# Kernel tuning notes

Measured on AMD Instinct MI355X. Metric: run time of the kernel, lower is better.

Reference implementation:

```python
import jax, jax.numpy as jnp
import numpy as np
from jax import lax

B, L, D, H, NW, NL = 4, 256, 768, 384, 4, 9
WINDOWS = (3, 5, 7, 9)


def setup_inputs() -> dict:
    key = jax.random.key(0)
    ks = jax.random.split(key, 12)
    s = 0.05
    return {
        "seq_out": jax.random.normal(ks[0], (B, L, D), jnp.float32),
        "valid_ids": jax.random.randint(ks[1], (B, L), 0, 2),
        "w_ih_f": jax.random.normal(ks[2], (NW, 4 * H, D), jnp.float32) * s,
        "w_hh_f": jax.random.normal(ks[3], (NW, 4 * H, H), jnp.float32) * s,
        "b_ih_f": jax.random.normal(ks[4], (NW, 4 * H), jnp.float32) * s,
        "b_hh_f": jax.random.normal(ks[5], (NW, 4 * H), jnp.float32) * s,
        "w_ih_b": jax.random.normal(ks[6], (NW, 4 * H, D), jnp.float32) * s,
        "w_hh_b": jax.random.normal(ks[7], (NW, 4 * H, H), jnp.float32) * s,
        "b_ih_b": jax.random.normal(ks[8], (NW, 4 * H), jnp.float32) * s,
        "b_hh_b": jax.random.normal(ks[9], (NW, 4 * H), jnp.float32) * s,
        "lin_w": jax.random.normal(ks[10], (NL, D), jnp.float32) * s,
        "lin_b": jnp.zeros((NL,), jnp.float32),
    }


def _lstm_last(win, mask, W_ih, W_hh, b, reverse):
    # invalid (out-of-range) steps leave the state untouched, so the final
    # carry equals the hidden state after the last valid step (PyTorch LSTM math).
    Bx, Lx, w, Dx = win.shape
    Hh = W_hh.shape[1]

    def step(carry, xm):
        h, c = carry
        x_t, m = xm  # [B,L,D], [L]
        gates = x_t @ W_ih.T + h @ W_hh.T + b  # [B,L,4H], gate order i,f,g,o
        i, f, g, o = jnp.split(gates, 4, axis=-1)
        i = jax.nn.sigmoid(i)
        f = jax.nn.sigmoid(f)
        g = jnp.tanh(g)
        o = jax.nn.sigmoid(o)
        c_new = f * c + i * g
        h_new = o * jnp.tanh(c_new)
        m3 = m[None, :, None]
        return (jnp.where(m3, h_new, h), jnp.where(m3, c_new, c)), None

    init = (jnp.zeros((Bx, Lx, Hh), win.dtype), jnp.zeros((Bx, Lx, Hh), win.dtype))
    (h, _), _ = lax.scan(step, init, (jnp.moveaxis(win, 2, 0), mask.T), reverse=reverse)
    return h


def _window_features(x, w, Wif, Whf, bf, Wib, Whb, bb):
    # Faithful vectorization of windows_sequence: the sorted index_list for
    # position i is the contiguous slice [max(0,i-w//2) .. min(L-1,i+w//2)].
    Bx, Lx, Dx = x.shape
    half = w // 2
    pos = jnp.arange(Lx)[:, None] + jnp.arange(-half, half + 1)[None, :]  # [L,w]
    mask = (pos >= 0) & (pos < Lx)
    idx = jnp.clip(pos, 0, Lx - 1)
    win = x[:, idx, :]  # [B,L,w,D]
    h_f = _lstm_last(win, mask, Wif, Whf, bf, reverse=False)  # fwd dir: last output
    h_b = _lstm_last(win, mask, Wib, Whb, bb, reverse=True)   # bwd dir over reversed window
    return jnp.concatenate([h_f, h_b], axis=-1)  # [B,L,D]


def _valid_scatter(x, valid_ids):
    # Left-pack tokens with valid_ids==1 (the nested Python scatter loop).
    Bx, Lx, Dx = x.shape
    v = valid_ids.astype(jnp.int32)
    dest = jnp.where(v == 1, jnp.cumsum(v, axis=1) - 1, Lx)  # invalid -> pad slot

    def pack(row_x, row_d):
        return jnp.zeros((Lx + 1, Dx), row_x.dtype).at[row_d].set(row_x)[:Lx]

    return jax.vmap(pack)(x, dest)


def reference(seq_out, valid_ids, w_ih_f, w_hh_f, b_ih_f, b_hh_f,
              w_ih_b, w_hh_b, b_ih_b, b_hh_b, lin_w, lin_b):
    x = _valid_scatter(seq_out, valid_ids)  # [B,L,D]; dropout is identity in eval
    locals_ = [
        _window_features(x, WINDOWS[i],
                         w_ih_f[i], w_hh_f[i], b_ih_f[i] + b_hh_f[i],
                         w_ih_b[i], w_hh_b[i], b_ih_b[i] + b_hh_b[i])
        for i in range(NW)
    ]
    muti = jnp.stack(locals_, axis=2)  # [B,L,NW,D]
    # dot-att: query is the (packed) sequence output itself
    attn = jax.nn.softmax(
        jnp.einsum('bld,blwd->blw', x, muti) / jnp.sqrt(jnp.float32(D)), axis=-1)
    local_feat = jnp.einsum('blw,blwd->bld', attn, muti)
    out = x + local_feat
    return out @ lin_w.T + lin_b  # logits [B,L,NL]
```

## Files before the change

kernel.cpp:

```cpp
#include <hip/hip_runtime.h>
#include <math.h>

#define LL 256
#define DD 768
#define HH 384
#define G4 1536
#define NWIN 4
#define NLIN 9
#define NPOS 1024
#define PROJ_N 12288
#define HSTRIDE 520

typedef __attribute__((ext_vector_type(8))) short short8;
typedef __attribute__((ext_vector_type(4))) short short4v;
typedef __attribute__((ext_vector_type(16))) float f32x16;

static __device__ __forceinline__ float bf2f(unsigned short u) {
    union { unsigned int i; float f; } v; v.i = ((unsigned int)u) << 16; return v.f;
}
static __device__ __forceinline__ unsigned short f2bf(float f) {
    unsigned int u = __float_as_uint(f);
    u += 0x7fff + ((u >> 16) & 1);
    return (unsigned short)(u >> 16);
}
static __device__ __forceinline__ float fsig(float x) {
    return __builtin_amdgcn_rcpf(1.f + __expf(-x));
}
static __device__ __forceinline__ float ftanh(float x) {
    return 1.f - 2.f * __builtin_amdgcn_rcpf(1.f + __expf(2.f * x));
}

__global__ void zero_f4(float4* __restrict__ p, int n4) {
    int i = blockIdx.x * blockDim.x + threadIdx.x;
    if (i < n4) p[i] = make_float4(0.f, 0.f, 0.f, 0.f);
}

__global__ void scatter_kernel(const float* __restrict__ seq,
                               const int* __restrict__ valid,
                               unsigned short* __restrict__ xfrag) {
    const int b = blockIdx.x >> 5;
    const int chunk = blockIdx.x & 31;
    const int tid = threadIdx.x;
    __shared__ int vbuf[LL];
    __shared__ int dest[LL];
    vbuf[tid] = valid[b * LL + tid];
    __syncthreads();
    if (tid == 0) {
        int c = 0;
        for (int l = 0; l < LL; ++l) dest[l] = vbuf[l] ? c++ : -1;
    }
    __syncthreads();
    for (int l = chunk * 8; l < chunk * 8 + 8; ++l) {
        const int d = dest[l];
        if (d >= 0) {
            const float* src = seq + (size_t)(b * LL + l) * DD;
            const int pos = b * LL + d;
            const int pt = pos >> 5, pl = pos & 31;
            for (int j = tid; j < DD / 8; j += 256) {
                const float4 v0 = ((const float4*)src)[2 * j];
                const float4 v1 = ((const float4*)src)[2 * j + 1];
                short8 pv;
                pv[0] = (short)f2bf(v0.x); pv[1] = (short)f2bf(v0.y);
                pv[2] = (short)f2bf(v0.z); pv[3] = (short)f2bf(v0.w);
                pv[4] = (short)f2bf(v1.x); pv[5] = (short)f2bf(v1.y);
                pv[6] = (short)f2bf(v1.z); pv[7] = (short)f2bf(v1.w);
                *(short8*)(xfrag + ((size_t)(pt * 48 + (j >> 1)) * 512 + (pl + 32 * (j & 1)) * 8)) = pv;
            }
        }
    }
}

__global__ __launch_bounds__(256) void cast_frag(
        const float* __restrict__ srcF, const float* __restrict__ srcB,
        unsigned short* __restrict__ dst, int K) {
    __shared__ unsigned short lds[32 * 768];
    const int tid = threadIdx.x;
    const int vrow0 = blockIdx.x * 32;
    const int chain = vrow0 / G4;
    const int dir = chain >> 2, wi = chain & 3;
    const float* src = (dir ? srcB : srcF) + (size_t)(wi * G4 + (vrow0 % G4)) * K;
    const int total = 32 * K;
    for (int i = tid * 4; i < total; i += 1024) {
        const float4 v = *(const float4*)(src + i);
        lds[i + 0] = f2bf(v.x); lds[i + 1] = f2bf(v.y);
        lds[i + 2] = f2bf(v.z); lds[i + 3] = f2bf(v.w);
    }
    __syncthreads();
    const int nks = K >> 4;
    for (int slot = tid; slot < nks * 64; slot += 256) {
        const int ks = slot >> 6;
        const int lane = slot & 63;
        const int row = lane & 31;
        const int kb = ks * 16 + (lane >> 5) * 8;
        const short8 v = *(const short8*)&lds[row * K + kb];
        *(short8*)(dst + ((size_t)blockIdx.x * nks + ks) * 512 + lane * 8) = v;
    }
}

__global__ __launch_bounds__(256) void proj_mfma(
        const unsigned short* __restrict__ xf,
        const unsigned short* __restrict__ wf,
        const float* __restrict__ bihf, const float* __restrict__ bhhf,
        const float* __restrict__ bihb, const float* __restrict__ bhhb,
        unsigned short* __restrict__ proj) {
    __shared__ __align__(16) unsigned short st[4 * 4096];
    const int wv = threadIdx.x >> 6;
    const int lane = threadIdx.x & 63;
    const int colid = lane & 31, hq = lane >> 5;
    const int chain = blockIdx.x & 7;
    const int r8 = blockIdx.x >> 3;
    const int us = r8 % 12;
    const int mtg = r8 / 12;
    const int dir = chain >> 2, wi = chain & 3;

    const unsigned short* bP = wf + (size_t)((chain * 48 + wv * 12 + us) * 48) * 512 + lane * 8;
    const unsigned short* aP = xf + (size_t)(mtg * 4 * 48) * 512 + lane * 8;

    f32x16 acc[4] = {};
#pragma unroll 4
    for (int ks = 0; ks < 48; ++ks) {
        const short8 bv = *(const short8*)(bP + ks * 512);
        const short8 a0 = *(const short8*)(aP + (0 * 48 + ks) * 512);
        const short8 a1 = *(const short8*)(aP + (1 * 48 + ks) * 512);
        const short8 a2 = *(const short8*)(aP + (2 * 48 + ks) * 512);
        const short8 a3 = *(const short8*)(aP + (3 * 48 + ks) * 512);
        acc[0] = __builtin_amdgcn_mfma_f32_32x32x16_bf16(a0, bv, acc[0], 0, 0, 0);
        acc[1] = __builtin_amdgcn_mfma_f32_32x32x16_bf16(a1, bv, acc[1], 0, 0, 0);
        acc[2] = __builtin_amdgcn_mfma_f32_32x32x16_bf16(a2, bv, acc[2], 0, 0, 0);
        acc[3] = __builtin_amdgcn_mfma_f32_32x32x16_bf16(a3, bv, acc[3], 0, 0, 0);
    }
    const int br = wv * HH + us * 32 + colid;
    const float bv = (dir ? bihb : bihf)[wi * G4 + br] + (dir ? bhhb : bhhf)[wi * G4 + br];
#pragma unroll
    for (int i = 0; i < 4; ++i) {
#pragma unroll
        for (int r = 0; r < 16; ++r) {
            const int row = (r & 3) + 8 * (r >> 2) + 4 * hq;
            st[i * 4096 + (row * 32 + colid) * 4 + wv] = f2bf(acc[i][r] + bv);
        }
    }
    __syncthreads();
#pragma unroll
    for (int j = 0; j < 8; ++j) {
        const int idx = j * 256 + threadIdx.x;
        const int i = idx >> 9, rem = idx & 511;
        const int pl = rem >> 4, q = rem & 15;
        const int pos = (mtg * 4 + i) * 32 + pl;
        *(int4*)(proj + (size_t)pos * PROJ_N + chain * G4 + us * 128 + q * 8) =
            ((const int4*)st)[idx];
    }
}

__global__ __launch_bounds__(768, 3) void lstm_fused(
        const unsigned short* __restrict__ Wf,
        const unsigned short* __restrict__ proj,
        unsigned short* __restrict__ hfin) {
    const int chain = blockIdx.x & 7;
    const int pt = blockIdx.x >> 3;
    const int dir = chain >> 2, wi = chain & 3;
    const int w = 3 + 2 * wi, half = wi + 1;
    const int tid = threadIdx.x;
    const int lane = tid & 63, wv = tid >> 6;
    const int colid = lane & 31, hq = lane >> 5;
    const int uu = wv * 32 + colid;
    const int m0 = pt * 32, b = m0 >> 8, l0 = m0 & 255;

    __shared__ __align__(16) unsigned short Hbuf[2][24 * HSTRIDE];
    float c[16];
#pragma unroll
    for (int r = 0; r < 16; ++r) c[r] = 0.f;

    const unsigned short* projb = proj + (size_t)(b * LL) * PROJ_N + chain * G4 + uu * 4;
    const unsigned short* Wb = Wf + (size_t)((chain * 48 + wv) * 24) * 512 + lane * 8;
    const int ksp = uu >> 4, khp = (uu >> 3) & 1, jp = uu & 7;
    const int hslot = ksp * HSTRIDE + khp * 256 + jp;

    for (int s = 0; s < w; ++s) {
        const int t = dir ? (w - 1 - s) : s;
        const int tmh = t - half;
        unsigned short* cur = Hbuf[s & 1];
        const unsigned short* prev = Hbuf[(s & 1) ^ 1];

        short4v pj[16];
#pragma unroll
        for (int r = 0; r < 16; ++r) {
            const int row = (r & 3) + 8 * (r >> 2) + 4 * hq;
            int src = l0 + row + tmh;
            src = src < 0 ? 0 : (src > LL - 1 ? LL - 1 : src);
            pj[r] = __builtin_nontemporal_load((const short4v*)(projb + src * PROJ_N));
        }

        f32x16 acc0 = {}, acc1 = {}, acc2 = {}, acc3 = {};
        if (s > 0) {
            const unsigned short* Alds = prev + lane * 8;
#pragma unroll 4
            for (int ks = 0; ks < 24; ++ks) {
                const short8 av  = *(const short8*)(Alds + ks * HSTRIDE);
                const short8 bv0 = *(const short8*)(Wb + (size_t)(0 * 288 + ks) * 512);
                const short8 bv1 = *(const short8*)(Wb + (size_t)(1 * 288 + ks) * 512);
                const short8 bv2 = *(const short8*)(Wb + (size_t)(2 * 288 + ks) * 512);
                const short8 bv3 = *(const short8*)(Wb + (size_t)(3 * 288 + ks) * 512);
                acc0 = __builtin_amdgcn_mfma_f32_32x32x16_bf16(av, bv0, acc0, 0, 0, 0);
                acc1 = __builtin_amdgcn_mfma_f32_32x32x16_bf16(av, bv1, acc1, 0, 0, 0);
                acc2 = __builtin_amdgcn_mfma_f32_32x32x16_bf16(av, bv2, acc2, 0, 0, 0);
                acc3 = __builtin_amdgcn_mfma_f32_32x32x16_bf16(av, bv3, acc3, 0, 0, 0);
            }
        }

#pragma unroll
        for (int r = 0; r < 16; ++r) {
            const int row = (r & 3) + 8 * (r >> 2) + 4 * hq;
            const int src = l0 + row + tmh;
            unsigned short hv;
            if (src >= 0 && src < LL) {
                const float gi = acc0[r] + bf2f((unsigned short)pj[r][0]);
                const float gf = acc1[r] + bf2f((unsigned short)pj[r][1]);
                const float gg = acc2[r] + bf2f((unsigned short)pj[r][2]);
                const float go = acc3[r] + bf2f((unsigned short)pj[r][3]);
                c[r] = fsig(gf) * c[r] + fsig(gi) * ftanh(gg);
                hv = f2bf(fsig(go) * ftanh(c[r]));
            } else {
                hv = (s == 0) ? (unsigned short)0 : prev[hslot + row * 8];
            }
            cur[hslot + row * 8] = hv;
        }
        __syncthreads();
    }

    const unsigned short* fin = Hbuf[(w - 1) & 1];
    unsigned short* ho = hfin + (size_t)chain * (NPOS * HH) + (size_t)pt * 12288;
#pragma unroll
    for (int i = tid; i < 1536; i += 768) {
        const int ks = i >> 6, off = i & 63;
        *(int4*)(ho + ks * 512 + off * 8) = *(const int4*)(fin + ks * HSTRIDE + off * 8);
    }
}

__global__ __launch_bounds__(512) void attn_out_kernel(
        const unsigned short* __restrict__ xfrag,
        const unsigned short* __restrict__ hfin,
        const float* __restrict__ lin_w, const float* __restrict__ lin_b,
        float* __restrict__ out) {
    const int pt = blockIdx.x;
    const int tid = threadIdx.x;
    const int lane = tid & 63, wv = tid >> 6;
    const int dir = wv >> 2, kr = wv & 3;
    const int pos = lane & 31, kh = lane >> 5;
    const float inv_sqrt_d = 0.03608439182435161f;

    __shared__ float scp[8][4][32];
    __shared__ float attw[4][32];
    __shared__ float redp[8][32][10];

    const unsigned short* xb = xfrag + ((size_t)(pt * 48 + 24 * dir)) * 512 + lane * 8;
    const unsigned short* hb0 = hfin + (size_t)(dir * 4) * (NPOS * HH) + (size_t)pt * 12288 + lane * 8;

    float sc4[4] = {0.f, 0.f, 0.f, 0.f};
#pragma unroll
    for (int k = 0; k < 6; ++k) {
        const int ks = kr * 6 + k;
        const short8 xv = *(const short8*)(xb + ks * 512);
        float xf[8];
#pragma unroll
        for (int j = 0; j < 8; ++j) xf[j] = bf2f((unsigned short)xv[j]);
#pragma unroll
        for (int wi = 0; wi < 4; ++wi) {
            const short8 hv = *(const short8*)(hb0 + (size_t)wi * (NPOS * HH) + ks * 512);
#pragma unroll
            for (int j = 0; j < 8; ++j)
                sc4[wi] = fmaf(xf[j], bf2f((unsigned short)hv[j]), sc4[wi]);
        }
    }
#pragma unroll
    for (int wi = 0; wi < 4; ++wi) sc4[wi] += __shfl_down(sc4[wi], 32);
    if (lane < 32) {
#pragma unroll
        for (int wi = 0; wi < 4; ++wi) scp[wv][wi][pos] = sc4[wi];
    }
    __syncthreads();
    if (tid < 32) {
        float s[4], mx = -1e30f;
#pragma unroll
        for (int wi = 0; wi < 4; ++wi) {
            float v = 0.f;
#pragma unroll
            for (int g = 0; g < 8; ++g) v += scp[g][wi][tid];
            s[wi] = v * inv_sqrt_d;
            mx = fmaxf(mx, s[wi]);
        }
        float denom = 0.f;
#pragma unroll
        for (int wi = 0; wi < 4; ++wi) { s[wi] = __expf(s[wi] - mx); denom += s[wi]; }
        const float rd = __builtin_amdgcn_rcpf(denom);
#pragma unroll
        for (int wi = 0; wi < 4; ++wi) attw[wi][tid] = s[wi] * rd;
    }
    __syncthreads();

    float aw[4];
#pragma unroll
    for (int wi = 0; wi < 4; ++wi) aw[wi] = attw[wi][pos];
    float rp[9];
#pragma unroll
    for (int r = 0; r < 9; ++r) rp[r] = 0.f;
#pragma unroll
    for (int k = 0; k < 6; ++k) {
        const int ks = kr * 6 + k;
        const short8 xv = *(const short8*)(xb + ks * 512);
        float ov[8];
#pragma unroll
        for (int j = 0; j < 8; ++j) ov[j] = bf2f((unsigned short)xv[j]);
#pragma unroll
        for (int wi = 0; wi < 4; ++wi) {
            const short8 hv = *(const short8*)(hb0 + (size_t)wi * (NPOS * HH) + ks * 512);
#pragma unroll
            for (int j = 0; j < 8; ++j)
                ov[j] = fmaf(aw[wi], bf2f((unsigned short)hv[j]), ov[j]);
        }
        const int dbase = dir * 384 + ks * 16 + kh * 8;
#pragma unroll
        for (int r = 0; r < 9; ++r) {
            const float4 lw0 = *(const float4*)(lin_w + r * DD + dbase);
            const float4 lw1 = *(const float4*)(lin_w + r * DD + dbase + 4);
            rp[r] += ov[0] * lw0.x + ov[1] * lw0.y + ov[2] * lw0.z + ov[3] * lw0.w
                   + ov[4] * lw1.x + ov[5] * lw1.y + ov[6] * lw1.z + ov[7] * lw1.w;
        }
    }
#pragma unroll
    for (int r = 0; r < 9; ++r) rp[r] += __shfl_down(rp[r], 32);
    if (lane < 32) {
#pragma unroll
        for (int r = 0; r < 9; ++r) redp[wv][pos][r] = rp[r];
    }
    __syncthreads();
    if (tid < 288) {
        const int p2 = tid / 9, r = tid % 9;
        float s = lin_b[r];
#pragma unroll
        for (int g = 0; g < 8; ++g) s += redp[g][p2][r];
        out[(size_t)(pt * 32 + p2) * NLIN + r] = s;
    }
}

extern "C" void kernel_launch(void* const* d_in, const int* in_sizes, int n_in,
                              void* d_out, int out_size, void* d_ws, size_t ws_size,
                              hipStream_t stream) {
    (void)in_sizes; (void)n_in; (void)out_size; (void)ws_size;
    const float* seq   = (const float*)d_in[0];
    const int*   valid = (const int*)d_in[1];
    const float* wih_f = (const float*)d_in[2];
    const float* whh_f = (const float*)d_in[3];
    const float* bih_f = (const float*)d_in[4];
    const float* bhh_f = (const float*)d_in[5];
    const float* wih_b = (const float*)d_in[6];
    const float* whh_b = (const float*)d_in[7];
    const float* bih_b = (const float*)d_in[8];
    const float* bhh_b = (const float*)d_in[9];
    const float* lin_w = (const float*)d_in[10];
    const float* lin_b = (const float*)d_in[11];
    float* out = (float*)d_out;

    unsigned short* xfrag = (unsigned short*)d_ws;
    unsigned short* proj  = xfrag + (size_t)NPOS * DD;
    unsigned short* wfhh  = proj + (size_t)NPOS * PROJ_N;
    unsigned short* wfih  = wfhh + (size_t)4718592;
    unsigned short* hfin  = wfih + (size_t)9437184;

    zero_f4<<<(98304 + 255) / 256, 256, 0, stream>>>((float4*)xfrag, 98304);
    scatter_kernel<<<128, 256, 0, stream>>>(seq, valid, xfrag);
    cast_frag<<<384, 256, 0, stream>>>(wih_f, wih_b, wfih, DD);
    cast_frag<<<384, 256, 0, stream>>>(whh_f, whh_b, wfhh, HH);
    proj_mfma<<<768, 256, 0, stream>>>(xfrag, wfih, bih_f, bhh_f, bih_b, bhh_b, proj);
    lstm_fused<<<256, 768, 0, stream>>>(wfhh, proj, hfin);
    attn_out_kernel<<<32, 512, 0, stream>>>(xfrag, hfin, lin_w, lin_b, out);
}
```

Baseline: 308.7 us.

## Software-pipeline recurrent weight loads and reorder LSTM block-to-chain mapping

Measured after the change: 525.4 us. 70.2% more time.

```diff
diff --git a/kernel.cpp b/kernel.cpp
--- a/kernel.cpp
+++ b/kernel.cpp
@@ -151,12 +151,36 @@
     }
 }
 
+#define LOADC(buf, c)                                                          \
+    {                                                                          \
+        _Pragma("unroll") for (int k2 = 0; k2 < 2; ++k2)                       \
+            _Pragma("unroll") for (int g = 0; g < 4; ++g)                      \
+                buf[k2 * 4 + g] = *(const short8*)(Wb +                        \
+                    (size_t)(g * 288 + (c) * 2 + k2) * 512);                   \
+    }
+
+#define CONSC(buf, c)                                                          \
+    {                                                                          \
+        _Pragma("unroll") for (int k2 = 0; k2 < 2; ++k2) {                     \
+            const short8 av = *(const short8*)(Alds + ((c) * 2 + k2) * HSTRIDE); \
+            acc0 = __builtin_amdgcn_mfma_f32_32x32x16_bf16(av, buf[k2 * 4 + 0], acc0, 0, 0, 0); \
+            acc1 = __builtin_amdgcn_mfma_f32_32x32x16_bf16(av, buf[k2 * 4 + 1], acc1, 0, 0, 0); \
+            acc2 = __builtin_amdgcn_mfma_f32_32x32x16_bf16(av, buf[k2 * 4 + 2], acc2, 0, 0, 0); \
+            acc3 = __builtin_amdgcn_mfma_f32_32x32x16_bf16(av, buf[k2 * 4 + 3], acc3, 0, 0, 0); \
+        }                                                                      \
+    }
+
 __global__ __launch_bounds__(768, 3) void lstm_fused(
         const unsigned short* __restrict__ Wf,
         const unsigned short* __restrict__ proj,
         unsigned short* __restrict__ hfin) {
-    const int chain = blockIdx.x & 7;
-    const int pt = blockIdx.x >> 3;
+    const int x = blockIdx.x & 7;
+    const int s0 = blockIdx.x >> 3;
+    const int pr = x >> 1;
+    int lc = (pr & 1) ? 7 : 3; if (pr & 2) lc -= 1;
+    int sc = ((pr & 1) ? 4 : 0) + ((pr & 2) ? 1 : 0);
+    const int chain = (s0 < 16) ? lc : sc;
+    const int pt = (x & 1) * 16 + (s0 & 15);
     const int dir = chain >> 2, wi = chain & 3;
     const int w = 3 + 2 * wi, half = wi + 1;
     const int tid = threadIdx.x;
@@ -175,12 +199,32 @@
     const int ksp = uu >> 4, khp = (uu >> 3) & 1, jp = uu & 7;
     const int hslot = ksp * HSTRIDE + khp * 256 + jp;
 
+    short8 wA[8], wB[8];
+    LOADC(wA, 0);
+
     for (int s = 0; s < w; ++s) {
         const int t = dir ? (w - 1 - s) : s;
         const int tmh = t - half;
         unsigned short* cur = Hbuf[s & 1];
         const unsigned short* prev = Hbuf[(s & 1) ^ 1];
 
+        f32x16 acc0 = {}, acc1 = {}, acc2 = {}, acc3 = {};
+        if (s > 0) {
+            const unsigned short* Alds = prev + lane * 8;
+            LOADC(wB, 1);  CONSC(wA, 0);
+            LOADC(wA, 2);  CONSC(wB, 1);
+            LOADC(wB, 3);  CONSC(wA, 2);
+            LOADC(wA, 4);  CONSC(wB, 3);
+            LOADC(wB, 5);  CONSC(wA, 4);
+            LOADC(wA, 6);  CONSC(wB, 5);
+            LOADC(wB, 7);  CONSC(wA, 6);
+            LOADC(wA, 8);  CONSC(wB, 7);
+            LOADC(wB, 9);  CONSC(wA, 8);
+            LOADC(wA, 10); CONSC(wB, 9);
+            LOADC(wB, 11); CONSC(wA, 10);
+            LOADC(wA, 0);  CONSC(wB, 11);
+        }
+
         short4v pj[16];
 #pragma unroll
         for (int r = 0; r < 16; ++r) {
@@ -188,23 +232,6 @@
             int src = l0 + row + tmh;
             src = src < 0 ? 0 : (src > LL - 1 ? LL - 1 : src);
             pj[r] = __builtin_nontemporal_load((const short4v*)(projb + src * PROJ_N));
-        }
-
-        f32x16 acc0 = {}, acc1 = {}, acc2 = {}, acc3 = {};
-        if (s > 0) {
-            const unsigned short* Alds = prev + lane * 8;
-#pragma unroll 4
-            for (int ks = 0; ks < 24; ++ks) {
-                const short8 av  = *(const short8*)(Alds + ks * HSTRIDE);
-                const short8 bv0 = *(const short8*)(Wb + (size_t)(0 * 288 + ks) * 512);
-                const short8 bv1 = *(const short8*)(Wb + (size_t)(1 * 288 + ks) * 512);
-                const short8 bv2 = *(const short8*)(Wb + (size_t)(2 * 288 + ks) * 512);
-                const short8 bv3 = *(const short8*)(Wb + (size_t)(3 * 288 + ks) * 512);
-                acc0 = __builtin_amdgcn_mfma_f32_32x32x16_bf16(av, bv0, acc0, 0, 0, 0);
-                acc1 = __builtin_amdgcn_mfma_f32_32x32x16_bf16(av, bv1, acc1, 0, 0, 0);
-                acc2 = __builtin_amdgcn_mfma_f32_32x32x16_bf16(av, bv2, acc2, 0, 0, 0);
-                acc3 = __builtin_amdgcn_mfma_f32_32x32x16_bf16(av, bv3, acc3, 0, 0, 0);
-            }
         }
 
 #pragma unroll
```

## Fuse prep kernels into one launch and reorder LSTM block-to-chain mapping

Applied to the files above, without the earlier changes.

Measured after the change: 290.0 us. 6.0% less time.

```diff
diff --git a/kernel.cpp b/kernel.cpp
--- a/kernel.cpp
+++ b/kernel.cpp
@@ -30,70 +30,83 @@
     return 1.f - 2.f * __builtin_amdgcn_rcpf(1.f + __expf(2.f * x));
 }
 
-__global__ void zero_f4(float4* __restrict__ p, int n4) {
-    int i = blockIdx.x * blockDim.x + threadIdx.x;
-    if (i < n4) p[i] = make_float4(0.f, 0.f, 0.f, 0.f);
-}
-
-__global__ void scatter_kernel(const float* __restrict__ seq,
-                               const int* __restrict__ valid,
-                               unsigned short* __restrict__ xfrag) {
-    const int b = blockIdx.x >> 5;
-    const int chunk = blockIdx.x & 31;
+__global__ __launch_bounds__(256) void prep_kernel(
+        const float* __restrict__ seq, const int* __restrict__ valid,
+        unsigned short* __restrict__ xfrag,
+        const float* __restrict__ wihF, const float* __restrict__ wihB,
+        unsigned short* __restrict__ wfih,
+        const float* __restrict__ whhF, const float* __restrict__ whhB,
+        unsigned short* __restrict__ wfhh) {
     const int tid = threadIdx.x;
-    __shared__ int vbuf[LL];
-    __shared__ int dest[LL];
-    vbuf[tid] = valid[b * LL + tid];
-    __syncthreads();
-    if (tid == 0) {
-        int c = 0;
-        for (int l = 0; l < LL; ++l) dest[l] = vbuf[l] ? c++ : -1;
-    }
-    __syncthreads();
-    for (int l = chunk * 8; l < chunk * 8 + 8; ++l) {
-        const int d = dest[l];
-        if (d >= 0) {
-            const float* src = seq + (size_t)(b * LL + l) * DD;
-            const int pos = b * LL + d;
-            const int pt = pos >> 5, pl = pos & 31;
-            for (int j = tid; j < DD / 8; j += 256) {
-                const float4 v0 = ((const float4*)src)[2 * j];
-                const float4 v1 = ((const float4*)src)[2 * j + 1];
-                short8 pv;
-                pv[0] = (short)f2bf(v0.x); pv[1] = (short)f2bf(v0.y);
-                pv[2] = (short)f2bf(v0.z); pv[3] = (short)f2bf(v0.w);
-                pv[4] = (short)f2bf(v1.x); pv[5] = (short)f2bf(v1.y);
-                pv[6] = (short)f2bf(v1.z); pv[7] = (short)f2bf(v1.w);
-                *(short8*)(xfrag + ((size_t)(pt * 48 + (j >> 1)) * 512 + (pl + 32 * (j & 1)) * 8)) = pv;
+    if (blockIdx.x < 128) {
+        const int b = blockIdx.x >> 5;
+        const int chunk = blockIdx.x & 31;
+        __shared__ int vbuf[LL];
+        __shared__ int dest[LL];
+        __shared__ int nvalid;
+        vbuf[tid] = valid[b * LL + tid];
+        __syncthreads();
+        if (tid == 0) {
+            int c = 0;
+            for (int l = 0; l < LL; ++l) dest[l] = vbuf[l] ? c++ : -1;
+            nvalid = c;
+        }
+        __syncthreads();
+        const int nv = nvalid;
+        for (int l = chunk * 8; l < chunk * 8 + 8; ++l) {
+            const int d = dest[l];
+            if (d >= 0) {
+                const float* src = seq + (size_t)(b * LL + l) * DD;
+                const int pos = b * LL + d;
+                const int pt = pos >> 5, pl = pos & 31;
+                for (int j = tid; j < DD / 8; j += 256) {
+                    const float4 v0 = ((const float4*)src)[2 * j];
+                    const float4 v1 = ((const float4*)src)[2 * j + 1];
+                    short8 pv;
+                    pv[0] = (short)f2bf(v0.x); pv[1] = (short)f2bf(v0.y);
+                    pv[2] = (short)f2bf(v0.z); pv[3] = (short)f2bf(v0.w);
+                    pv[4] = (short)f2bf(v1.x); pv[5] = (short)f2bf(v1.y);
+                    pv[6] = (short)f2bf(v1.z); pv[7] = (short)f2bf(v1.w);
+                    *(short8*)(xfrag + ((size_t)(pt * 48 + (j >> 1)) * 512 + (pl + 32 * (j & 1)) * 8)) = pv;
+                }
             }
-        }
-    }
-}
-
-__global__ __launch_bounds__(256) void cast_frag(
-        const float* __restrict__ srcF, const float* __restrict__ srcB,
-        unsigned short* __restrict__ dst, int K) {
-    __shared__ unsigned short lds[32 * 768];
-    const int tid = threadIdx.x;
-    const int vrow0 = blockIdx.x * 32;
-    const int chain = vrow0 / G4;
-    const int dir = chain >> 2, wi = chain & 3;
-    const float* src = (dir ? srcB : srcF) + (size_t)(wi * G4 + (vrow0 % G4)) * K;
-    const int total = 32 * K;
-    for (int i = tid * 4; i < total; i += 1024) {
-        const float4 v = *(const float4*)(src + i);
-        lds[i + 0] = f2bf(v.x); lds[i + 1] = f2bf(v.y);
-        lds[i + 2] = f2bf(v.z); lds[i + 3] = f2bf(v.w);
-    }
-    __syncthreads();
-    const int nks = K >> 4;
-    for (int slot = tid; slot < nks * 64; slot += 256) {
-        const int ks = slot >> 6;
-        const int lane = slot & 63;
-        const int row = lane & 31;
-        const int kb = ks * 16 + (lane >> 5) * 8;
-        const short8 v = *(const short8*)&lds[row * K + kb];
-        *(short8*)(dst + ((size_t)blockIdx.x * nks + ks) * 512 + lane * 8) = v;
+            if (l >= nv) {
+                const int pos = b * LL + l;
+                const int pt = pos >> 5, pl = pos & 31;
+                const short8 zv = {};
+                for (int j = tid; j < DD / 8; j += 256)
+                    *(short8*)(xfrag + ((size_t)(pt * 48 + (j >> 1)) * 512 + (pl + 32 * (j & 1)) * 8)) = zv;
+            }
+        }
+    } else {
+        __shared__ unsigned short lds[32 * 768];
+        const int cb = blockIdx.x - 128;
+        const int isIH = cb < 384;
+        const int vblk = isIH ? cb : (cb - 384);
+        const int K = isIH ? DD : HH;
+        const float* srcF = isIH ? wihF : whhF;
+        const float* srcB = isIH ? wihB : whhB;
+        unsigned short* dst = isIH ? wfih : wfhh;
+        const int vrow0 = vblk * 32;
+        const int chain = vrow0 / G4;
+        const int dir = chain >> 2, wi = chain & 3;
+        const float* src = (dir ? srcB : srcF) + (size_t)(wi * G4 + (vrow0 % G4)) * K;
+        const int total = 32 * K;
+        for (int i = tid * 4; i < total; i += 1024) {
+            const float4 v = *(const float4*)(src + i);
+            lds[i + 0] = f2bf(v.x); lds[i + 1] = f2bf(v.y);
+            lds[i + 2] = f2bf(v.z); lds[i + 3] = f2bf(v.w);
+        }
+        __syncthreads();
+        const int nks = K >> 4;
+        for (int slot = tid; slot < nks * 64; slot += 256) {
+            const int ks = slot >> 6;
+            const int lane = slot & 63;
+            const int row = lane & 31;
+            const int kb = ks * 16 + (lane >> 5) * 8;
+            const short8 v = *(const short8*)&lds[row * K + kb];
+            *(short8*)(dst + ((size_t)vblk * nks + ks) * 512 + lane * 8) = v;
+        }
     }
 }
 
@@ -155,8 +168,12 @@
         const unsigned short* __restrict__ Wf,
         const unsigned short* __restrict__ proj,
         unsigned short* __restrict__ hfin) {
-    const int chain = blockIdx.x & 7;
-    const int pt = blockIdx.x >> 3;
+    const int p = blockIdx.x & 3, sub = (blockIdx.x >> 2) & 1;
+    const int slot = blockIdx.x >> 3;
+    const int chainA[4] = {3, 7, 2, 6};
+    const int chainB[4] = {0, 4, 1, 5};
+    const int chain = (slot < 16) ? chainA[p] : chainB[p];
+    const int pt = sub * 16 + (slot & 15);
     const int dir = chain >> 2, wi = chain & 3;
     const int w = 3 + 2 * wi, half = wi + 1;
     const int tid = threadIdx.x;
@@ -366,10 +383,9 @@
     unsigned short* wfih  = wfhh + (size_t)4718592;
     unsigned short* hfin  = wfih + (size_t)9437184;
 
-    zero_f4<<<(98304 + 255) / 256, 256, 0, stream>>>((float4*)xfrag, 98304);
-    scatter_kernel<<<128, 256, 0, stream>>>(seq, valid, xfrag);
-    cast_frag<<<384, 256, 0, stream>>>(wih_f, wih_b, wfih, DD);
-    cast_frag<<<384, 256, 0, stream>>>(whh_f, whh_b, wfhh, HH);
+    prep_kernel<<<896, 256, 0, stream>>>(seq, valid, xfrag,
+                                         wih_f, wih_b, wfih,
+                                         whh_f, whh_b, wfhh);
     proj_mfma<<<768, 256, 0, stream>>>(xfrag, wfih, bih_f, bhh_f, bih_b, bhh_b, proj);
     lstm_fused<<<256, 768, 0, stream>>>(wfhh, proj, hfin);
     attn_out_kernel<<<32, 512, 0, stream>>>(xfrag, hfin, lin_w, lin_b, out);
```
